# Kernel tuning notes

Hardware: AMD Instinct MI355X
Metric: run time of the kernel (lower is better)

Reference implementation:

```python
import jax, jax.numpy as jnp
import numpy as np

GRID = 192
ISO = 0.0

CORNERS = [(0,0,0),(1,0,0),(0,1,0),(1,1,0),(0,0,1),(1,0,1),(0,1,1),(1,1,1)]
# 12 cube edges as pairs of corner offsets
EDGES = [
    ((0,0,0),(1,0,0)),((0,1,0),(1,1,0)),((0,0,1),(1,0,1)),((0,1,1),(1,1,1)),
    ((0,0,0),(0,1,0)),((1,0,0),(1,1,0)),((0,0,1),(0,1,1)),((1,0,1),(1,1,1)),
    ((0,0,0),(0,0,1)),((1,0,0),(1,0,1)),((0,1,0),(0,1,1)),((1,1,0),(1,1,1)),
]


def setup_inputs() -> dict:
    key = jax.random.key(0)
    grid = jax.random.normal(key, (GRID, GRID, GRID), dtype=jnp.float32)
    return {"grid": grid}


def _dual_verts(grid, iso):
    # One dual vertex per cell of the padded grid: mean of the iso-crossing
    # points on the cell's 12 edges (dual-marching-cubes vertex placement).
    X, Y, Z = grid.shape
    P = jnp.pad(grid, 1, constant_values=iso + 1.0)  # (X+2, Y+2, Z+2)
    Cx, Cy, Cz = X + 1, Y + 1, Z + 1                 # number of cells per axis
    vals = {c: P[c[0]:c[0]+Cx, c[1]:c[1]+Cy, c[2]:c[2]+Cz] for c in CORNERS}
    sum_pt = jnp.zeros((Cx, Cy, Cz, 3), grid.dtype)
    cnt = jnp.zeros((Cx, Cy, Cz), grid.dtype)
    for ca, cb in EDGES:  # fixed 12-iteration loop, fully vectorized over cells
        vA, vB = vals[ca], vals[cb]
        m = (vA < iso) != (vB < iso)                 # edge crosses isosurface
        t = jnp.where(m, (iso - vA) / jnp.where(m, vB - vA, 1.0), 0.0)
        oa = jnp.asarray(ca, grid.dtype)
        ob = jnp.asarray(cb, grid.dtype)
        pt = oa + t[..., None] * (ob - oa)           # local crossing point
        mf = m.astype(grid.dtype)
        sum_pt = sum_pt + mf[..., None] * pt
        cnt = cnt + mf
    base = jnp.stack(jnp.meshgrid(jnp.arange(Cx), jnp.arange(Cy), jnp.arange(Cz), indexing='ij'), axis=-1).astype(grid.dtype)
    verts = base + sum_pt / jnp.maximum(cnt, 1.0)[..., None]
    # undo +1 padding offset, then normalize by (dim - 1) as in the module
    verts = (verts - 1.0) / (jnp.asarray([X, Y, Z], grid.dtype) - 1.0)
    return verts.reshape(-1, 3), (cnt > 0).reshape(-1)


def _quads(grid, iso):
    # One quad per grid edge that crosses the isosurface, connecting the dual
    # vertices of the 4 cells sharing that edge. Emitted densely with a mask
    # (jit-compatible fixed shapes); masked rows are inactive.
    X, Y, Z = grid.shape
    P = jnp.pad(grid, 1, constant_values=iso + 1.0)
    Cx, Cy, Cz = X + 1, Y + 1, Z + 1
    sgn = P < iso
    def cid(a, b, c):  # flatten cell index
        return (a * Cy + b) * Cz + c
    qs, ms = [], []
    # x-directed edges: shared by cells (i, j-1/j, k-1/k)
    m = sgn[0:Cx, 1:Cy, 1:Cz] != sgn[1:Cx+1, 1:Cy, 1:Cz]
    a = jnp.arange(Cx)[:, None, None]; b = jnp.arange(1, Cy)[None, :, None]; c = jnp.arange(1, Cz)[None, None, :]
    q = jnp.stack(jnp.broadcast_arrays(cid(a, b-1, c-1), cid(a, b, c-1), cid(a, b, c), cid(a, b-1, c)), axis=-1)
    qs.append(q.reshape(-1, 4)); ms.append(m.reshape(-1))
    # y-directed edges: shared by cells (i-1/i, j, k-1/k)
    m = sgn[1:Cx, 0:Cy, 1:Cz] != sgn[1:Cx, 1:Cy+1, 1:Cz]
    a = jnp.arange(1, Cx)[:, None, None]; b = jnp.arange(Cy)[None, :, None]; c = jnp.arange(1, Cz)[None, None, :]
    q = jnp.stack(jnp.broadcast_arrays(cid(a-1, b, c-1), cid(a, b, c-1), cid(a, b, c), cid(a-1, b, c)), axis=-1)
    qs.append(q.reshape(-1, 4)); ms.append(m.reshape(-1))
    # z-directed edges: shared by cells (i-1/i, j-1/j, k)
    m = sgn[1:Cx, 1:Cy, 0:Cz] != sgn[1:Cx, 1:Cy, 1:Cz+1]
    a = jnp.arange(1, Cx)[:, None, None]; b = jnp.arange(1, Cy)[None, :, None]; c = jnp.arange(Cz)[None, None, :]
    q = jnp.stack(jnp.broadcast_arrays(cid(a-1, b-1, c), cid(a, b-1, c), cid(a, b, c), cid(a-1, b, c)), axis=-1)
    qs.append(q.reshape(-1, 4)); ms.append(m.reshape(-1))
    quads = jnp.concatenate(qs, axis=0).astype(jnp.int32)
    qmask = jnp.concatenate(ms, axis=0)
    return quads, qmask


def reference(grid):
    verts, vmask = _dual_verts(grid, ISO)
    quads, qmask = _quads(grid, ISO)
    return verts, vmask, quads, qmask
```

## Files before the change

### kernel.cpp

```cpp
#include <hip/hip_runtime.h>

#define GN 192
#define CN 193
#define CN2 (CN * CN)

#define NV        ((size_t)CN * CN * CN)
#define OFF_VMASK ((size_t)(NV * 3))
#define OFF_QUADS ((size_t)(OFF_VMASK + NV))
#define QSEG      ((size_t)CN * GN * GN)
#define OFF_QMASK ((size_t)(OFF_QUADS + 3 * QSEG * 4))

typedef float f4 __attribute__((ext_vector_type(4)));

__device__ __forceinline__ void nts(float* p, float v) {
    __builtin_nontemporal_store(v, p);
}
__device__ __forceinline__ void nts4(f4* p, f4 v) {
    __builtin_nontemporal_store(v, p);
}

__device__ __forceinline__ float gpad(const float* __restrict__ g, int x, int y, int z) {
    if ((unsigned)x < (unsigned)GN && (unsigned)y < (unsigned)GN && (unsigned)z < (unsigned)GN)
        return g[((size_t)x * GN + y) * GN + z];
    return 1.0f;
}

__global__ __launch_bounds__(256) void dmc_fused(const float* __restrict__ g,
                                                 float* __restrict__ out) {
    __shared__ float vlds[256 * 3];

    const int tid = threadIdx.x;
    const size_t blockBase = (size_t)blockIdx.x * 256;
    const size_t lin = blockBase + tid;
    const bool valid = lin < NV;

    const int linI = (int)lin;
    const int k = linI % CN;
    const int t2 = linI / CN;
    const int j = t2 % CN;
    const int i = t2 / CN;

    float v000 = 1.f, v100 = 1.f, v010 = 1.f, v110 = 1.f;
    float v001 = 1.f, v101 = 1.f, v011 = 1.f, v111 = 1.f;
    if (valid) {
        const bool interior = ((unsigned)(i - 1) < (unsigned)(GN - 1)) &
                              ((unsigned)(j - 1) < (unsigned)(GN - 1)) &
                              ((unsigned)(k - 1) < (unsigned)(GN - 1));
        if (interior) {
            const float* b = g + ((size_t)(i - 1) * GN + (j - 1)) * GN + (k - 1);
            v000 = b[0];
            v001 = b[1];
            v010 = b[GN];
            v011 = b[GN + 1];
            v100 = b[GN * GN];
            v101 = b[GN * GN + 1];
            v110 = b[GN * GN + GN];
            v111 = b[GN * GN + GN + 1];
        } else {
            v000 = gpad(g, i - 1, j - 1, k - 1);
            v100 = gpad(g, i,     j - 1, k - 1);
            v010 = gpad(g, i - 1, j,     k - 1);
            v110 = gpad(g, i,     j,     k - 1);
            v001 = gpad(g, i - 1, j - 1, k);
            v101 = gpad(g, i,     j - 1, k);
            v011 = gpad(g, i - 1, j,     k);
            v111 = gpad(g, i,     j,     k);
        }
    }

    const bool s000 = v000 < 0.f, s100 = v100 < 0.f, s010 = v010 < 0.f, s110 = v110 < 0.f;
    const bool s001 = v001 < 0.f, s101 = v101 < 0.f, s011 = v011 < 0.f, s111 = v111 < 0.f;

    float sx = 0.f, sy = 0.f, sz = 0.f, cf = 0.f;
    auto acc = [&](float vA, float vB, bool sA, bool sB, int axis, float o1, float o2) {
        const bool c = sA != sB;
        const float m = c ? 1.0f : 0.0f;
        const float t = c ? (-vA * __builtin_amdgcn_rcpf(vB - vA)) : 0.0f;
        if (axis == 0)      { sx += t;      sy += m * o1; sz += m * o2; }
        else if (axis == 1) { sx += m * o1; sy += t;      sz += m * o2; }
        else                { sx += m * o1; sy += m * o2; sz += t;      }
        cf += m;
    };
    acc(v000, v100, s000, s100, 0, 0.f, 0.f);
    acc(v010, v110, s010, s110, 0, 1.f, 0.f);
    acc(v001, v101, s001, s101, 0, 0.f, 1.f);
    acc(v011, v111, s011, s111, 0, 1.f, 1.f);
    acc(v000, v010, s000, s010, 1, 0.f, 0.f);
    acc(v100, v110, s100, s110, 1, 1.f, 0.f);
    acc(v001, v011, s001, s011, 1, 0.f, 1.f);
    acc(v101, v111, s101, s111, 1, 1.f, 1.f);
    acc(v000, v001, s000, s001, 2, 0.f, 0.f);
    acc(v100, v101, s100, s101, 2, 1.f, 0.f);
    acc(v010, v011, s010, s011, 2, 0.f, 1.f);
    acc(v110, v111, s110, s111, 2, 1.f, 1.f);

    const float rc = __builtin_amdgcn_rcpf(fmaxf(cf, 1.0f));
    const float inv191 = 1.0f / 191.0f;

    vlds[tid * 3 + 0] = ((float)i + sx * rc - 1.0f) * inv191;
    vlds[tid * 3 + 1] = ((float)j + sy * rc - 1.0f) * inv191;
    vlds[tid * 3 + 2] = ((float)k + sz * rc - 1.0f) * inv191;
    __syncthreads();

    {
        const size_t gbase = blockBase * 3;
#pragma unroll
        for (int c = 0; c < 3; ++c) {
            const size_t idx = (size_t)tid + 256 * c;
            if (gbase + idx < NV * 3) nts(out + gbase + idx, vlds[idx]);
        }
    }

    if (valid) nts(out + OFF_VMASK + lin, (cf > 0.f) ? 1.0f : 0.0f);

    const float flin = (float)linI;
    f4* const quads = (f4*)(out + OFF_QUADS);
    float* const qmask = out + OFF_QMASK;

    if (valid && j < GN && k < GN) {
        const size_t r = ((size_t)i * GN + j) * GN + k;
        f4 q;
        q.x = flin;
        q.y = flin + (float)CN;
        q.z = flin + (float)(CN + 1);
        q.w = flin + 1.0f;
        nts4(quads + r, q);
        nts(qmask + r, (s011 != s111) ? 1.0f : 0.0f);
    }
    if (valid && i >= 1 && k < GN) {
        const size_t r = QSEG + ((size_t)(i - 1) * CN + j) * GN + k;
        f4 q;
        q.x = flin - (float)CN2;
        q.y = flin;
        q.z = flin + 1.0f;
        q.w = flin - (float)(CN2 - 1);
        nts4(quads + r, q);
        nts(qmask + r, (s001 != s011) ? 1.0f : 0.0f);
    }
    if (valid && i >= 1 && j >= 1) {
        const size_t r = 2 * QSEG + ((size_t)(i - 1) * GN + (j - 1)) * CN + k;
        f4 q;
        q.x = flin - (float)(CN2 + CN);
        q.y = flin - (float)CN;
        q.z = flin;
        q.w = flin - (float)CN2;
        nts4(quads + r, q);
        nts(qmask + r, (s000 != s001) ? 1.0f : 0.0f);
    }
}

extern "C" void kernel_launch(void* const* d_in, const int* in_sizes, int n_in,
                              void* d_out, int out_size, void* d_ws, size_t ws_size,
                              hipStream_t stream) {
    const float* g = (const float*)d_in[0];
    float* out = (float*)d_out;
    const int nblocks = (int)((NV + 255) / 256);
    dmc_fused<<<dim3(nblocks), dim3(256), 0, stream>>>(g, out);
}
```

Before: 572.7 us.

## Process four z-cells per thread with vectorized loads and stores

Each thread now handles four consecutive cells along z (193 = 48 groups of 4 plus an overlapping tail group). It loads four f4 columns plus one scalar each from the input instead of eight scalar loads per cell, and writes vertices, masks and quads with 16-byte vector stores, some of them unaligned. This removes the LDS staging and __syncthreads, cuts redundant input loads, and reduces the number of store instructions. The cost is more complex index logic and tail handling, overlapping writes in the tail group, and unaligned vector stores whose efficiency depends on the hardware.

```diff
diff --git a/kernel.cpp b/kernel.cpp
--- a/kernel.cpp
+++ b/kernel.cpp
@@ -10,7 +10,11 @@
 #define QSEG      ((size_t)CN * GN * GN)
 #define OFF_QMASK ((size_t)(OFF_QUADS + 3 * QSEG * 4))
 
+#define GPR 49
+#define NGRP ((size_t)CN2 * GPR)
+
 typedef float f4 __attribute__((ext_vector_type(4)));
+typedef f4 f4u __attribute__((aligned(4)));
 
 __device__ __forceinline__ void nts(float* p, float v) {
     __builtin_nontemporal_store(v, p);
@@ -18,134 +22,148 @@
 __device__ __forceinline__ void nts4(f4* p, f4 v) {
     __builtin_nontemporal_store(v, p);
 }
-
-__device__ __forceinline__ float gpad(const float* __restrict__ g, int x, int y, int z) {
-    if ((unsigned)x < (unsigned)GN && (unsigned)y < (unsigned)GN && (unsigned)z < (unsigned)GN)
-        return g[((size_t)x * GN + y) * GN + z];
-    return 1.0f;
+__device__ __forceinline__ void nts4u(float* p, f4 v) {
+    __builtin_nontemporal_store(v, (f4u*)p);
 }
 
-__global__ __launch_bounds__(256) void dmc_fused(const float* __restrict__ g,
-                                                 float* __restrict__ out) {
-    __shared__ float vlds[256 * 3];
+__global__ __launch_bounds__(256) void dmc4(const float* __restrict__ g,
+                                            float* __restrict__ out) {
+    const size_t gidx = (size_t)blockIdx.x * 256 + threadIdx.x;
+    const bool valid = gidx < NGRP;
+    const int gi = valid ? (int)gidx : (int)(NGRP - 1);
 
-    const int tid = threadIdx.x;
-    const size_t blockBase = (size_t)blockIdx.x * 256;
-    const size_t lin = blockBase + tid;
-    const bool valid = lin < NV;
+    const int row = gi / GPR;
+    const int kg  = gi - row * GPR;
+    const int i   = row / CN;
+    const int j   = row - i * CN;
+    const bool tail = (kg == 48);
+    const int K0 = tail ? 189 : 4 * kg;
 
-    const int linI = (int)lin;
-    const int k = linI % CN;
-    const int t2 = linI / CN;
-    const int j = t2 % CN;
-    const int i = t2 / CN;
+    const int zv = tail ? 188 : 4 * kg;
+    const int zs = (kg == 0) ? 0 : K0 - 1;
+    const int xc[2] = { (i >= 1) ? i - 1 : 0, (i <= GN - 1) ? i : GN - 1 };
+    const int yc[2] = { (j >= 1) ? j - 1 : 0, (j <= GN - 1) ? j : GN - 1 };
+    const bool xvld[2] = { i >= 1, i <= GN - 1 };
+    const bool yvld[2] = { j >= 1, j <= GN - 1 };
 
-    float v000 = 1.f, v100 = 1.f, v010 = 1.f, v110 = 1.f;
-    float v001 = 1.f, v101 = 1.f, v011 = 1.f, v111 = 1.f;
-    if (valid) {
-        const bool interior = ((unsigned)(i - 1) < (unsigned)(GN - 1)) &
-                              ((unsigned)(j - 1) < (unsigned)(GN - 1)) &
-                              ((unsigned)(k - 1) < (unsigned)(GN - 1));
-        if (interior) {
-            const float* b = g + ((size_t)(i - 1) * GN + (j - 1)) * GN + (k - 1);
-            v000 = b[0];
-            v001 = b[1];
-            v010 = b[GN];
-            v011 = b[GN + 1];
-            v100 = b[GN * GN];
-            v101 = b[GN * GN + 1];
-            v110 = b[GN * GN + GN];
-            v111 = b[GN * GN + GN + 1];
-        } else {
-            v000 = gpad(g, i - 1, j - 1, k - 1);
-            v100 = gpad(g, i,     j - 1, k - 1);
-            v010 = gpad(g, i - 1, j,     k - 1);
-            v110 = gpad(g, i,     j,     k - 1);
-            v001 = gpad(g, i - 1, j - 1, k);
-            v101 = gpad(g, i,     j - 1, k);
-            v011 = gpad(g, i - 1, j,     k);
-            v111 = gpad(g, i,     j,     k);
+    float w[4][5];
+#pragma unroll
+    for (int x = 0; x < 2; ++x) {
+#pragma unroll
+        for (int y = 0; y < 2; ++y) {
+            const float* b = g + ((size_t)xc[x] * GN + yc[y]) * GN;
+            const float s = b[zs];
+            const f4 V = *(const f4*)(b + zv);
+            const bool pv = xvld[x] & yvld[y];
+            float w0, w1, w2, w3, w4;
+            if (tail) { w0 = V.x; w1 = V.y; w2 = V.z; w3 = V.w; w4 = 1.0f; }
+            else      { w0 = (kg == 0) ? 1.0f : s; w1 = V.x; w2 = V.y; w3 = V.z; w4 = V.w; }
+            const int p = x * 2 + y;
+            w[p][0] = pv ? w0 : 1.0f;
+            w[p][1] = pv ? w1 : 1.0f;
+            w[p][2] = pv ? w2 : 1.0f;
+            w[p][3] = pv ? w3 : 1.0f;
+            w[p][4] = pv ? w4 : 1.0f;
         }
     }
 
-    const bool s000 = v000 < 0.f, s100 = v100 < 0.f, s010 = v010 < 0.f, s110 = v110 < 0.f;
-    const bool s001 = v001 < 0.f, s101 = v101 < 0.f, s011 = v011 < 0.f, s111 = v111 < 0.f;
+    float vb[12], vm[4], qa[4], qb[4], qc[4];
+    const float inv191 = 1.0f / 191.0f;
+#pragma unroll
+    for (int c = 0; c < 4; ++c) {
+        const float v000 = w[0][c], v001 = w[0][c + 1];
+        const float v010 = w[1][c], v011 = w[1][c + 1];
+        const float v100 = w[2][c], v101 = w[2][c + 1];
+        const float v110 = w[3][c], v111 = w[3][c + 1];
 
-    float sx = 0.f, sy = 0.f, sz = 0.f, cf = 0.f;
-    auto acc = [&](float vA, float vB, bool sA, bool sB, int axis, float o1, float o2) {
-        const bool c = sA != sB;
-        const float m = c ? 1.0f : 0.0f;
-        const float t = c ? (-vA * __builtin_amdgcn_rcpf(vB - vA)) : 0.0f;
-        if (axis == 0)      { sx += t;      sy += m * o1; sz += m * o2; }
-        else if (axis == 1) { sx += m * o1; sy += t;      sz += m * o2; }
-        else                { sx += m * o1; sy += m * o2; sz += t;      }
-        cf += m;
-    };
-    acc(v000, v100, s000, s100, 0, 0.f, 0.f);
-    acc(v010, v110, s010, s110, 0, 1.f, 0.f);
-    acc(v001, v101, s001, s101, 0, 0.f, 1.f);
-    acc(v011, v111, s011, s111, 0, 1.f, 1.f);
-    acc(v000, v010, s000, s010, 1, 0.f, 0.f);
-    acc(v100, v110, s100, s110, 1, 1.f, 0.f);
-    acc(v001, v011, s001, s011, 1, 0.f, 1.f);
-    acc(v101, v111, s101, s111, 1, 1.f, 1.f);
-    acc(v000, v001, s000, s001, 2, 0.f, 0.f);
-    acc(v100, v101, s100, s101, 2, 1.f, 0.f);
-    acc(v010, v011, s010, s011, 2, 0.f, 1.f);
-    acc(v110, v111, s110, s111, 2, 1.f, 1.f);
+        float sx = 0.f, sy = 0.f, sz = 0.f, cf = 0.f;
+        auto acc = [&](float vA, float vB, int axis, float o1, float o2) {
+            const bool cr = (vA < 0.f) != (vB < 0.f);
+            const float m = cr ? 1.0f : 0.0f;
+            const float t = cr ? (-vA * __builtin_amdgcn_rcpf(vB - vA)) : 0.0f;
+            if (axis == 0)      { sx += t;      sy += m * o1; sz += m * o2; }
+            else if (axis == 1) { sx += m * o1; sy += t;      sz += m * o2; }
+            else                { sx += m * o1; sy += m * o2; sz += t;      }
+            cf += m;
+        };
+        acc(v000, v100, 0, 0.f, 0.f);
+        acc(v010, v110, 0, 1.f, 0.f);
+        acc(v001, v101, 0, 0.f, 1.f);
+        acc(v011, v111, 0, 1.f, 1.f);
+        acc(v000, v010, 1, 0.f, 0.f);
+        acc(v100, v110, 1, 1.f, 0.f);
+        acc(v001, v011, 1, 0.f, 1.f);
+        acc(v101, v111, 1, 1.f, 1.f);
+        acc(v000, v001, 2, 0.f, 0.f);
+        acc(v100, v101, 2, 1.f, 0.f);
+        acc(v010, v011, 2, 0.f, 1.f);
+        acc(v110, v111, 2, 1.f, 1.f);
 
-    const float rc = __builtin_amdgcn_rcpf(fmaxf(cf, 1.0f));
-    const float inv191 = 1.0f / 191.0f;
+        const float rc = __builtin_amdgcn_rcpf(fmaxf(cf, 1.0f));
+        vb[c * 3 + 0] = ((float)i + sx * rc - 1.0f) * inv191;
+        vb[c * 3 + 1] = ((float)j + sy * rc - 1.0f) * inv191;
+        vb[c * 3 + 2] = ((float)(K0 + c) + sz * rc - 1.0f) * inv191;
+        vm[c] = (cf > 0.f) ? 1.0f : 0.0f;
+        qa[c] = ((v011 < 0.f) != (v111 < 0.f)) ? 1.0f : 0.0f;
+        qb[c] = ((v001 < 0.f) != (v011 < 0.f)) ? 1.0f : 0.0f;
+        qc[c] = ((v000 < 0.f) != (v001 < 0.f)) ? 1.0f : 0.0f;
+    }
 
-    vlds[tid * 3 + 0] = ((float)i + sx * rc - 1.0f) * inv191;
-    vlds[tid * 3 + 1] = ((float)j + sy * rc - 1.0f) * inv191;
-    vlds[tid * 3 + 2] = ((float)k + sz * rc - 1.0f) * inv191;
-    __syncthreads();
+    if (!valid) return;
+
+    const int lin0 = row * CN + K0;
+    const float flin = (float)lin0;
 
     {
-        const size_t gbase = blockBase * 3;
-#pragma unroll
-        for (int c = 0; c < 3; ++c) {
-            const size_t idx = (size_t)tid + 256 * c;
-            if (gbase + idx < NV * 3) nts(out + gbase + idx, vlds[idx]);
-        }
+        float* vp = out + (size_t)lin0 * 3;
+        nts4u(vp + 0, (f4){ vb[0], vb[1], vb[2],  vb[3] });
+        nts4u(vp + 4, (f4){ vb[4], vb[5], vb[6],  vb[7] });
+        nts4u(vp + 8, (f4){ vb[8], vb[9], vb[10], vb[11] });
     }
+    nts4u(out + OFF_VMASK + lin0, (f4){ vm[0], vm[1], vm[2], vm[3] });
 
-    if (valid) nts(out + OFF_VMASK + lin, (cf > 0.f) ? 1.0f : 0.0f);
-
-    const float flin = (float)linI;
     f4* const quads = (f4*)(out + OFF_QUADS);
     float* const qmask = out + OFF_QMASK;
 
-    if (valid && j < GN && k < GN) {
-        const size_t r = ((size_t)i * GN + j) * GN + k;
-        f4 q;
-        q.x = flin;
-        q.y = flin + (float)CN;
-        q.z = flin + (float)(CN + 1);
-        q.w = flin + 1.0f;
-        nts4(quads + r, q);
-        nts(qmask + r, (s011 != s111) ? 1.0f : 0.0f);
+    if (j < GN) {
+        const size_t r = ((size_t)i * GN + j) * GN + K0;
+        nts4(quads + r + 0, (f4){ flin + 0.f, flin + 193.f, flin + 194.f, flin + 1.f });
+        nts4(quads + r + 1, (f4){ flin + 1.f, flin + 194.f, flin + 195.f, flin + 2.f });
+        nts4(quads + r + 2, (f4){ flin + 2.f, flin + 195.f, flin + 196.f, flin + 3.f });
+        if (!tail) {
+            nts4(quads + r + 3, (f4){ flin + 3.f, flin + 196.f, flin + 197.f, flin + 4.f });
+            nts4u(qmask + r, (f4){ qa[0], qa[1], qa[2], qa[3] });
+        } else {
+            nts(qmask + r + 0, qa[0]);
+            nts(qmask + r + 1, qa[1]);
+            nts(qmask + r + 2, qa[2]);
+        }
     }
-    if (valid && i >= 1 && k < GN) {
-        const size_t r = QSEG + ((size_t)(i - 1) * CN + j) * GN + k;
-        f4 q;
-        q.x = flin - (float)CN2;
-        q.y = flin;
-        q.z = flin + 1.0f;
-        q.w = flin - (float)(CN2 - 1);
-        nts4(quads + r, q);
-        nts(qmask + r, (s001 != s011) ? 1.0f : 0.0f);
+    if (i >= 1) {
+        const size_t r = QSEG + ((size_t)(i - 1) * CN + j) * GN + K0;
+        const float dB = -(float)CN2;
+        nts4(quads + r + 0, (f4){ flin + dB + 0.f, flin + 0.f, flin + 1.f, flin + dB + 1.f });
+        nts4(quads + r + 1, (f4){ flin + dB + 1.f, flin + 1.f, flin + 2.f, flin + dB + 2.f });
+        nts4(quads + r + 2, (f4){ flin + dB + 2.f, flin + 2.f, flin + 3.f, flin + dB + 3.f });
+        if (!tail) {
+            nts4(quads + r + 3, (f4){ flin + dB + 3.f, flin + 3.f, flin + 4.f, flin + dB + 4.f });
+            nts4u(qmask + QSEG + ((size_t)(i - 1) * CN + j) * GN + K0 - QSEG + r - r + r, (f4){ qb[0], qb[1], qb[2], qb[3] });
+        } else {
+            nts(qmask + r + 0, qb[0]);
+            nts(qmask + r + 1, qb[1]);
+            nts(qmask + r + 2, qb[2]);
+        }
     }
-    if (valid && i >= 1 && j >= 1) {
-        const size_t r = 2 * QSEG + ((size_t)(i - 1) * GN + (j - 1)) * CN + k;
-        f4 q;
-        q.x = flin - (float)(CN2 + CN);
-        q.y = flin - (float)CN;
-        q.z = flin;
-        q.w = flin - (float)CN2;
-        nts4(quads + r, q);
-        nts(qmask + r, (s000 != s001) ? 1.0f : 0.0f);
+    if (i >= 1 && j >= 1) {
+        const size_t r = 2 * QSEG + ((size_t)(i - 1) * GN + (j - 1)) * CN + K0;
+        const float d0 = -(float)(CN2 + CN);
+        const float d1 = -(float)CN;
+        const float d3 = -(float)CN2;
+        nts4(quads + r + 0, (f4){ flin + d0 + 0.f, flin + d1 + 0.f, flin + 0.f, flin + d3 + 0.f });
+        nts4(quads + r + 1, (f4){ flin + d0 + 1.f, flin + d1 + 1.f, flin + 1.f, flin + d3 + 1.f });
+        nts4(quads + r + 2, (f4){ flin + d0 + 2.f, flin + d1 + 2.f, flin + 2.f, flin + d3 + 2.f });
+        nts4(quads + r + 3, (f4){ flin + d0 + 3.f, flin + d1 + 3.f, flin + 3.f, flin + d3 + 3.f });
+        nts4u(qmask + r, (f4){ qc[0], qc[1], qc[2], qc[3] });
     }
 }
 
@@ -154,6 +172,6 @@
                               hipStream_t stream) {
     const float* g = (const float*)d_in[0];
     float* out = (float*)d_out;
-    const int nblocks = (int)((NV + 255) / 256);
-    dmc_fused<<<dim3(nblocks), dim3(256), 0, stream>>>(g, out);
+    const int nblocks = (int)((NGRP + 255) / 256);
+    dmc4<<<dim3(nblocks), dim3(256), 0, stream>>>(g, out);
 }
```

Result: slower. 1.035 ms (+80.7%).

## Split quad index writes into separate coalesced kernel and compact mask stores via LDS

Applied to the files above, without the earlier changes.

Splits the fused kernel in two. A dedicated kernel writes the constant quad-index table with fully contiguous float4 stores. The vertex kernel stages its quad masks in shared memory and writes them as contiguous runs, and stores vertices as float4. This removes the scattered, uncoalesced quad and qmask stores of the fused kernel, at the cost of a second launch and extra index arithmetic. It also replaces the boundary branches with clamped, predicated loads and adds a Newton refinement step to each reciprocal.

```diff
diff --git a/kernel.cpp b/kernel.cpp
--- a/kernel.cpp
+++ b/kernel.cpp
@@ -12,141 +12,161 @@
 
 typedef float f4 __attribute__((ext_vector_type(4)));
 
-__device__ __forceinline__ void nts(float* p, float v) {
-    __builtin_nontemporal_store(v, p);
-}
-__device__ __forceinline__ void nts4(f4* p, f4 v) {
-    __builtin_nontemporal_store(v, p);
+__device__ __forceinline__ void nts(float* p, float v) { __builtin_nontemporal_store(v, p); }
+__device__ __forceinline__ void nts4(f4* p, f4 v) { __builtin_nontemporal_store(v, p); }
+
+#define QBLK 6948
+
+__global__ __launch_bounds__(256) void dmc_quads(float* __restrict__ out) {
+    f4* const quads = (f4*)(out + OFF_QUADS);
+    const unsigned b = blockIdx.x;
+    const unsigned seg = b / QBLK;
+    const unsigned r0 = (b - seg * QBLK) * 1024u + threadIdx.x;
+    float d0, d1, d2, d3;
+    if (seg == 0)      { d0 = 0.f;      d1 = 193.f;  d2 = 194.f; d3 = 1.f; }
+    else if (seg == 1) { d0 = -37249.f; d1 = 0.f;    d2 = 1.f;   d3 = -37248.f; }
+    else               { d0 = -37442.f; d1 = -193.f; d2 = 0.f;   d3 = -37249.f; }
+#pragma unroll
+    for (int s = 0; s < 4; ++s) {
+        const unsigned r = r0 + 256u * s;
+        unsigned i, j, k, t;
+        if (seg == 0)      { k = r % GN; t = r / GN; j = t % GN; i = t / GN; }
+        else if (seg == 1) { k = r % GN; t = r / GN; j = t % CN; i = t / CN + 1; }
+        else               { k = r % CN; t = r / CN; j = t % GN + 1; i = t / GN + 1; }
+        const float flin = (float)((i * CN + j) * CN + k);
+        nts4(quads + seg * QSEG + r, (f4){flin + d0, flin + d1, flin + d2, flin + d3});
+    }
 }
 
-__device__ __forceinline__ float gpad(const float* __restrict__ g, int x, int y, int z) {
-    if ((unsigned)x < (unsigned)GN && (unsigned)y < (unsigned)GN && (unsigned)z < (unsigned)GN)
-        return g[((size_t)x * GN + y) * GN + z];
-    return 1.0f;
-}
-
-__global__ __launch_bounds__(256) void dmc_fused(const float* __restrict__ g,
+__global__ __launch_bounds__(256) void dmc_verts(const float* __restrict__ g,
                                                  float* __restrict__ out) {
-    __shared__ float vlds[256 * 3];
+    __shared__ __align__(16) float vlds[256 * 3];
+    __shared__ float qAl[256], qBl[256], qCl[256];
 
     const int tid = threadIdx.x;
-    const size_t blockBase = (size_t)blockIdx.x * 256;
-    const size_t lin = blockBase + tid;
+    const size_t lin0 = (size_t)blockIdx.x * 256;
+    const size_t lin = lin0 + tid;
     const bool valid = lin < NV;
-
-    const int linI = (int)lin;
+    const int linI = valid ? (int)lin : (int)(NV - 1);
     const int k = linI % CN;
     const int t2 = linI / CN;
     const int j = t2 % CN;
     const int i = t2 / CN;
 
-    float v000 = 1.f, v100 = 1.f, v010 = 1.f, v110 = 1.f;
-    float v001 = 1.f, v101 = 1.f, v011 = 1.f, v111 = 1.f;
-    if (valid) {
-        const bool interior = ((unsigned)(i - 1) < (unsigned)(GN - 1)) &
-                              ((unsigned)(j - 1) < (unsigned)(GN - 1)) &
-                              ((unsigned)(k - 1) < (unsigned)(GN - 1));
-        if (interior) {
-            const float* b = g + ((size_t)(i - 1) * GN + (j - 1)) * GN + (k - 1);
-            v000 = b[0];
-            v001 = b[1];
-            v010 = b[GN];
-            v011 = b[GN + 1];
-            v100 = b[GN * GN];
-            v101 = b[GN * GN + 1];
-            v110 = b[GN * GN + GN];
-            v111 = b[GN * GN + GN + 1];
-        } else {
-            v000 = gpad(g, i - 1, j - 1, k - 1);
-            v100 = gpad(g, i,     j - 1, k - 1);
-            v010 = gpad(g, i - 1, j,     k - 1);
-            v110 = gpad(g, i,     j,     k - 1);
-            v001 = gpad(g, i - 1, j - 1, k);
-            v101 = gpad(g, i,     j - 1, k);
-            v011 = gpad(g, i - 1, j,     k);
-            v111 = gpad(g, i,     j,     k);
-        }
-    }
+    const int L0 = (int)lin0;
+    const int L1 = (int)((lin0 + 255 < NV) ? (lin0 + 255) : (NV - 1));
+    const int k0 = L0 % CN, u0 = L0 / CN, j0 = u0 % CN, i0 = u0 / CN;
+    const int k1 = L1 % CN, u1 = L1 / CN, j1 = u1 % CN, i1 = u1 / CN;
 
-    const bool s000 = v000 < 0.f, s100 = v100 < 0.f, s010 = v010 < 0.f, s110 = v110 < 0.f;
-    const bool s001 = v001 < 0.f, s101 = v101 < 0.f, s011 = v011 < 0.f, s111 = v111 < 0.f;
+    int rminA, rmaxA, rminB, rmaxB, rminC, rmaxC;
+    { int a = i0, bb = j0, c = k0;
+      if (bb == GN) { a++; bb = 0; c = 0; }
+      else if (c == GN) { bb++; c = 0; if (bb == GN) { a++; bb = 0; } }
+      rminA = (a * GN + bb) * GN + c; }
+    { int a = i1, bb = j1, c = k1;
+      if (bb == GN) { bb = GN - 1; c = GN - 1; }
+      else if (c == GN) { c = GN - 1; }
+      rmaxA = (a * GN + bb) * GN + c; }
+    { int a = i0, bb = j0, c = k0;
+      if (a == 0) { a = 1; bb = 0; c = 0; }
+      else if (c == GN) { bb++; c = 0; if (bb == CN) { bb = 0; a++; } }
+      rminB = ((a - 1) * CN + bb) * GN + c; }
+    { int a = i1, bb = j1, c = k1;
+      if (a == 0) rmaxB = -1;
+      else { if (c == GN) c = GN - 1; rmaxB = ((a - 1) * CN + bb) * GN + c; } }
+    { int a = i0, bb = j0, c = k0;
+      if (a == 0) { a = 1; bb = 1; c = 0; }
+      else if (bb == 0) { bb = 1; c = 0; }
+      rminC = ((a - 1) * GN + (bb - 1)) * CN + c; }
+    { int a = i1, bb = j1, c = k1;
+      if (a == 0) rmaxC = -1;
+      else if (bb == 0) { a--; rmaxC = (a == 0) ? -1 : ((a - 1) * GN + (GN - 1)) * CN + (CN - 1); }
+      else rmaxC = ((a - 1) * GN + (bb - 1)) * CN + c; }
+    int cntA = rmaxA - rminA + 1; if (cntA < 0) cntA = 0;
+    int cntB = rmaxB - rminB + 1; if (cntB < 0) cntB = 0;
+    int cntC = rmaxC - rminC + 1; if (cntC < 0) cntC = 0;
+
+    const int xm = (i >= 1) ? i - 1 : 0;
+    const int xp = (i <= GN - 1) ? i : GN - 1;
+    const int ym = (j >= 1) ? j - 1 : 0;
+    const int yp = (j <= GN - 1) ? j : GN - 1;
+    const int zm = (k >= 1) ? k - 1 : 0;
+    const int zp = (k <= GN - 1) ? k : GN - 1;
+    const bool xv0 = (i >= 1), xv1 = (i <= GN - 1);
+    const bool yv0 = (j >= 1), yv1 = (j <= GN - 1);
+    const bool zv0 = (k >= 1), zv1 = (k <= GN - 1);
+
+    const float* b00 = g + ((size_t)xm * GN + ym) * GN;
+    const float* b01 = g + ((size_t)xm * GN + yp) * GN;
+    const float* b10 = g + ((size_t)xp * GN + ym) * GN;
+    const float* b11 = g + ((size_t)xp * GN + yp) * GN;
+
+    const float v000 = (xv0 & yv0 & zv0) ? b00[zm] : 1.0f;
+    const float v001 = (xv0 & yv0 & zv1) ? b00[zp] : 1.0f;
+    const float v010 = (xv0 & yv1 & zv0) ? b01[zm] : 1.0f;
+    const float v011 = (xv0 & yv1 & zv1) ? b01[zp] : 1.0f;
+    const float v100 = (xv1 & yv0 & zv0) ? b10[zm] : 1.0f;
+    const float v101 = (xv1 & yv0 & zv1) ? b10[zp] : 1.0f;
+    const float v110 = (xv1 & yv1 & zv0) ? b11[zm] : 1.0f;
+    const float v111 = (xv1 & yv1 & zv1) ? b11[zp] : 1.0f;
 
     float sx = 0.f, sy = 0.f, sz = 0.f, cf = 0.f;
-    auto acc = [&](float vA, float vB, bool sA, bool sB, int axis, float o1, float o2) {
-        const bool c = sA != sB;
-        const float m = c ? 1.0f : 0.0f;
-        const float t = c ? (-vA * __builtin_amdgcn_rcpf(vB - vA)) : 0.0f;
+    auto acc = [&](float vA, float vB, int axis, float o1, float o2) {
+        const bool cr = (vA < 0.f) != (vB < 0.f);
+        const float m = cr ? 1.0f : 0.0f;
+        const float d = cr ? (vB - vA) : 1.0f;
+        float r = __builtin_amdgcn_rcpf(d);
+        r = r * (2.0f - d * r);
+        const float t = cr ? (-vA * r) : 0.0f;
         if (axis == 0)      { sx += t;      sy += m * o1; sz += m * o2; }
         else if (axis == 1) { sx += m * o1; sy += t;      sz += m * o2; }
         else                { sx += m * o1; sy += m * o2; sz += t;      }
         cf += m;
     };
-    acc(v000, v100, s000, s100, 0, 0.f, 0.f);
-    acc(v010, v110, s010, s110, 0, 1.f, 0.f);
-    acc(v001, v101, s001, s101, 0, 0.f, 1.f);
-    acc(v011, v111, s011, s111, 0, 1.f, 1.f);
-    acc(v000, v010, s000, s010, 1, 0.f, 0.f);
-    acc(v100, v110, s100, s110, 1, 1.f, 0.f);
-    acc(v001, v011, s001, s011, 1, 0.f, 1.f);
-    acc(v101, v111, s101, s111, 1, 1.f, 1.f);
-    acc(v000, v001, s000, s001, 2, 0.f, 0.f);
-    acc(v100, v101, s100, s101, 2, 1.f, 0.f);
-    acc(v010, v011, s010, s011, 2, 0.f, 1.f);
-    acc(v110, v111, s110, s111, 2, 1.f, 1.f);
+    acc(v000, v100, 0, 0.f, 0.f);
+    acc(v010, v110, 0, 1.f, 0.f);
+    acc(v001, v101, 0, 0.f, 1.f);
+    acc(v011, v111, 0, 1.f, 1.f);
+    acc(v000, v010, 1, 0.f, 0.f);
+    acc(v100, v110, 1, 1.f, 0.f);
+    acc(v001, v011, 1, 0.f, 1.f);
+    acc(v101, v111, 1, 1.f, 1.f);
+    acc(v000, v001, 2, 0.f, 0.f);
+    acc(v100, v101, 2, 1.f, 0.f);
+    acc(v010, v011, 2, 0.f, 1.f);
+    acc(v110, v111, 2, 1.f, 1.f);
 
-    const float rc = __builtin_amdgcn_rcpf(fmaxf(cf, 1.0f));
+    const float cfm = fmaxf(cf, 1.0f);
+    float rc = __builtin_amdgcn_rcpf(cfm);
+    rc = rc * (2.0f - cfm * rc);
     const float inv191 = 1.0f / 191.0f;
-
     vlds[tid * 3 + 0] = ((float)i + sx * rc - 1.0f) * inv191;
     vlds[tid * 3 + 1] = ((float)j + sy * rc - 1.0f) * inv191;
     vlds[tid * 3 + 2] = ((float)k + sz * rc - 1.0f) * inv191;
-    __syncthreads();
-
-    {
-        const size_t gbase = blockBase * 3;
-#pragma unroll
-        for (int c = 0; c < 3; ++c) {
-            const size_t idx = (size_t)tid + 256 * c;
-            if (gbase + idx < NV * 3) nts(out + gbase + idx, vlds[idx]);
-        }
-    }
 
     if (valid) nts(out + OFF_VMASK + lin, (cf > 0.f) ? 1.0f : 0.0f);
 
-    const float flin = (float)linI;
-    f4* const quads = (f4*)(out + OFF_QUADS);
-    float* const qmask = out + OFF_QMASK;
+    if (valid) {
+        if (j < GN && k < GN)
+            qAl[(i * GN + j) * GN + k - rminA] = ((v011 < 0.f) != (v111 < 0.f)) ? 1.0f : 0.0f;
+        if (i >= 1 && k < GN)
+            qBl[((i - 1) * CN + j) * GN + k - rminB] = ((v001 < 0.f) != (v011 < 0.f)) ? 1.0f : 0.0f;
+        if (i >= 1 && j >= 1)
+            qCl[((i - 1) * GN + (j - 1)) * CN + k - rminC] = ((v000 < 0.f) != (v001 < 0.f)) ? 1.0f : 0.0f;
+    }
+    __syncthreads();
 
-    if (valid && j < GN && k < GN) {
-        const size_t r = ((size_t)i * GN + j) * GN + k;
-        f4 q;
-        q.x = flin;
-        q.y = flin + (float)CN;
-        q.z = flin + (float)(CN + 1);
-        q.w = flin + 1.0f;
-        nts4(quads + r, q);
-        nts(qmask + r, (s011 != s111) ? 1.0f : 0.0f);
-    }
-    if (valid && i >= 1 && k < GN) {
-        const size_t r = QSEG + ((size_t)(i - 1) * CN + j) * GN + k;
-        f4 q;
-        q.x = flin - (float)CN2;
-        q.y = flin;
-        q.z = flin + 1.0f;
-        q.w = flin - (float)(CN2 - 1);
-        nts4(quads + r, q);
-        nts(qmask + r, (s001 != s011) ? 1.0f : 0.0f);
-    }
-    if (valid && i >= 1 && j >= 1) {
-        const size_t r = 2 * QSEG + ((size_t)(i - 1) * GN + (j - 1)) * CN + k;
-        f4 q;
-        q.x = flin - (float)(CN2 + CN);
-        q.y = flin - (float)CN;
-        q.z = flin;
-        q.w = flin - (float)CN2;
-        nts4(quads + r, q);
-        nts(qmask + r, (s000 != s001) ? 1.0f : 0.0f);
-    }
+    const int nvalid = L1 - L0 + 1;
+    const int nfl = 3 * nvalid;
+    const int nf4 = nfl >> 2;
+    if (tid < nf4)
+        nts4((f4*)(out + lin0 * 3) + tid, ((const f4*)vlds)[tid]);
+    if (tid == nf4)
+        for (int rr = nf4 * 4; rr < nfl; ++rr) nts(out + lin0 * 3 + rr, vlds[rr]);
+
+    if (tid < cntA) nts(out + OFF_QMASK + (size_t)rminA + tid, qAl[tid]);
+    if (tid < cntB) nts(out + OFF_QMASK + QSEG + (size_t)rminB + tid, qBl[tid]);
+    if (tid < cntC) nts(out + OFF_QMASK + 2 * QSEG + (size_t)rminC + tid, qCl[tid]);
 }
 
 extern "C" void kernel_launch(void* const* d_in, const int* in_sizes, int n_in,
@@ -154,6 +174,7 @@
                               hipStream_t stream) {
     const float* g = (const float*)d_in[0];
     float* out = (float*)d_out;
-    const int nblocks = (int)((NV + 255) / 256);
-    dmc_fused<<<dim3(nblocks), dim3(256), 0, stream>>>(g, out);
+    const int nbV = (int)((NV + 255) / 256);
+    dmc_verts<<<dim3(nbV), dim3(256), 0, stream>>>(g, out);
+    dmc_quads<<<dim3(3 * QBLK), dim3(256), 0, stream>>>(out);
 }
```

After: 573.5 us. About the same (+0.1%).
